# Kernel optimization log

Measured on AMD Instinct MI355X. Metric: run time of the kernel, lower is better.

Reference implementation:

```python
import jax, jax.numpy as jnp
import numpy as np

SAMPLE_RATE = 44100.0
MIN_GAIN, MAX_GAIN = -12.0, 12.0
MIN_Q, MAX_Q = 0.1, 10.0
# (min, max) for the 15 normalized control params, in channel order
PARAM_RANGES = np.array([
    (MIN_GAIN, MAX_GAIN), (20.0, 2000.0), (MIN_Q, MAX_Q),      # low shelf
    (MIN_GAIN, MAX_GAIN), (20.0, 200.0), (MIN_Q, MAX_Q),       # band0 peaking
    (MIN_GAIN, MAX_GAIN), (200.0, 2000.0), (MIN_Q, MAX_Q),     # band1 peaking
    (MIN_GAIN, MAX_GAIN), (2000.0, 12000.0), (MIN_Q, MAX_Q),   # band2 peaking
    (MIN_GAIN, MAX_GAIN), (4000.0, 16000.0), (MIN_Q, MAX_Q),   # high shelf
], dtype=np.float32)


def _biquad(gain_db, f0, q, ftype):
    """RBJ cookbook biquad. Inputs shape (bs,), returns (bs, 6) normalized so a0==1."""
    A = 10.0 ** (gain_db / 40.0)
    w0 = 2.0 * jnp.pi * (f0 / SAMPLE_RATE)
    alpha = jnp.sin(w0) / (2.0 * q)
    cw = jnp.cos(w0)
    sA = jnp.sqrt(A)
    if ftype == 'peaking':
        b0 = 1.0 + alpha * A; b1 = -2.0 * cw; b2 = 1.0 - alpha * A
        a0 = 1.0 + alpha / A; a1 = -2.0 * cw; a2 = 1.0 - alpha / A
    elif ftype == 'low_shelf':
        b0 = A * ((A + 1) - (A - 1) * cw + 2 * sA * alpha)
        b1 = 2 * A * ((A - 1) - (A + 1) * cw)
        b2 = A * ((A + 1) - (A - 1) * cw - 2 * sA * alpha)
        a0 = (A + 1) + (A - 1) * cw + 2 * sA * alpha
        a1 = -2 * ((A - 1) + (A + 1) * cw)
        a2 = (A + 1) + (A - 1) * cw - 2 * sA * alpha
    else:  # high_shelf
        b0 = A * ((A + 1) + (A - 1) * cw + 2 * sA * alpha)
        b1 = -2 * A * ((A - 1) + (A + 1) * cw)
        b2 = A * ((A + 1) + (A - 1) * cw - 2 * sA * alpha)
        a0 = (A + 1) - (A - 1) * cw + 2 * sA * alpha
        a1 = 2 * ((A - 1) - (A + 1) * cw)
        a2 = (A + 1) - (A - 1) * cw - 2 * sA * alpha
    coeffs = jnp.stack([b0, b1, b2, a0, a1, a2], axis=-1)
    return coeffs / a0[..., None]


def _compute_sos(p):
    """p: (bs, 15) denormalized params -> sos (bs, 5, 6)."""
    secs = [
        _biquad(p[:, 0], p[:, 1], p[:, 2], 'low_shelf'),
        _biquad(p[:, 3], p[:, 4], p[:, 5], 'peaking'),
        _biquad(p[:, 6], p[:, 7], p[:, 8], 'peaking'),
        _biquad(p[:, 9], p[:, 10], p[:, 11], 'peaking'),
        _biquad(p[:, 12], p[:, 13], p[:, 14], 'high_shelf'),
    ]
    return jnp.stack(secs, axis=1)


def _sosfilt(sos, x):
    """Cascaded 5-section biquad, direct form II transposed, zero initial state.
    sos: (bs, 5, 6), x: (bs, T) -> (bs, T)."""
    b0, b1, b2 = sos[..., 0], sos[..., 1], sos[..., 2]  # each (bs, 5)
    a1, a2 = sos[..., 4], sos[..., 5]

    def step(carry, xt):
        z1, z2 = carry  # (bs, 5) each
        s = xt  # (bs,)
        z1n, z2n = [], []
        for k in range(5):  # fixed small cascade
            y = b0[:, k] * s + z1[:, k]
            z1n.append(b1[:, k] * s - a1[:, k] * y + z2[:, k])
            z2n.append(b2[:, k] * s - a2[:, k] * y)
            s = y
        return (jnp.stack(z1n, 1), jnp.stack(z2n, 1)), s

    bs = x.shape[0]
    z0 = jnp.zeros((bs, 5), x.dtype)
    _, y = jax.lax.scan(step, (z0, z0), x.T)
    return y.T


def setup_inputs() -> dict:
    key = jax.random.key(0)
    k1, k2 = jax.random.split(key)
    x = jax.random.normal(k1, (32, 1, 131072), dtype=jnp.float32)
    control_params = jax.random.uniform(k2, (32, 15, 1), dtype=jnp.float32)
    return {"x": x, "control_params": control_params}


def reference(x, control_params):
    # denormalize: min + p * (max - min)
    lo = jnp.asarray(PARAM_RANGES[:, 0])
    hi = jnp.asarray(PARAM_RANGES[:, 1])
    p = control_params[:, :, 0]  # (bs, 15)
    p_denorm = lo[None, :] + p * (hi - lo)[None, :]
    sos = _compute_sos(p_denorm)           # (bs, 5, 6)
    y = _sosfilt(sos, x[:, 0, :])          # (bs, T)
    return y[:, None, :], sos
```

## Files before the change

### kernel.cpp

```cpp
#include <hip/hip_runtime.h>
#include <math.h>


#define NB 32
#define LCH 16
#define T_LEN 131072
#define CPB 256
#define BPB 32
#define CCH 8192
#define WPB 128
#define NPOW 13

__constant__ double c_lo[15] = {-12.0,   20.0, 0.1,
                                -12.0,   20.0, 0.1,
                                -12.0,  200.0, 0.1,
                                -12.0, 2000.0, 0.1,
                                -12.0, 4000.0, 0.1};
__constant__ double c_hi[15] = { 12.0,  2000.0, 10.0,
                                 12.0,   200.0, 10.0,
                                 12.0,  2000.0, 10.0,
                                 12.0, 12000.0, 10.0,
                                 12.0, 16000.0, 10.0};

__global__ __launch_bounds__(128)
void eq_setup(const float* __restrict__ cp, float* __restrict__ sos_out,
              float* __restrict__ powers)
{
    int b = blockIdx.x;
    int t = threadIdx.x;
    __shared__ float  sc[5][5];
    __shared__ double Abuf[2][10][10];

    if (t < 5) {
        int k = t;
        double p[3];
#pragma unroll
        for (int j = 0; j < 3; ++j) {
            int i = k * 3 + j;
            double pv = (double)cp[b * 15 + i];
            p[j] = c_lo[i] + pv * (c_hi[i] - c_lo[i]);
        }
        double A     = exp(p[0] * (M_LN10 / 40.0));
        double w0    = 2.0 * M_PI * p[1] / 44100.0;
        double alpha = sin(w0) / (2.0 * p[2]);
        double cw    = cos(w0);
        double sA    = sqrt(A);
        double b0, b1, b2, a0, a1, a2;
        if (k == 0) {
            b0 =     A * ((A + 1) - (A - 1) * cw + 2 * sA * alpha);
            b1 = 2 * A * ((A - 1) - (A + 1) * cw);
            b2 =     A * ((A + 1) - (A - 1) * cw - 2 * sA * alpha);
            a0 =          (A + 1) + (A - 1) * cw + 2 * sA * alpha;
            a1 =    -2 * ((A - 1) + (A + 1) * cw);
            a2 =          (A + 1) + (A - 1) * cw - 2 * sA * alpha;
        } else if (k == 4) {
            b0 =     A * ((A + 1) + (A - 1) * cw + 2 * sA * alpha);
            b1 = -2 * A * ((A - 1) + (A + 1) * cw);
            b2 =     A * ((A + 1) + (A - 1) * cw - 2 * sA * alpha);
            a0 =          (A + 1) - (A - 1) * cw + 2 * sA * alpha;
            a1 =     2 * ((A - 1) - (A + 1) * cw);
            a2 =          (A + 1) - (A - 1) * cw - 2 * sA * alpha;
        } else {
            b0 = 1.0 + alpha * A;
            b1 = -2.0 * cw;
            b2 = 1.0 - alpha * A;
            a0 = 1.0 + alpha / A;
            a1 = -2.0 * cw;
            a2 = 1.0 - alpha / A;
        }
        double inv = 1.0 / a0;
        float fb0 = (float)(b0 * inv), fb1 = (float)(b1 * inv), fb2 = (float)(b2 * inv);
        float fa1 = (float)(a1 * inv), fa2 = (float)(a2 * inv);
        float* o = sos_out + (size_t)(b * 5 + k) * 6;
        o[0] = fb0; o[1] = fb1; o[2] = fb2; o[3] = 1.0f; o[4] = fa1; o[5] = fa2;
        sc[k][0] = fb0; sc[k][1] = fb1; sc[k][2] = fb2; sc[k][3] = fa1; sc[k][4] = fa2;
    }
    __syncthreads();

    if (t < 10) {
        double z[10];
#pragma unroll
        for (int i = 0; i < 10; ++i) z[i] = 0.0;
        z[t] = 1.0;
        double s = 0.0;
        double zn[10];
#pragma unroll
        for (int k = 0; k < 5; ++k) {
            double b0 = sc[k][0], b1 = sc[k][1], b2 = sc[k][2];
            double a1 = sc[k][3], a2 = sc[k][4];
            double y = b0 * s + z[2 * k];
            zn[2 * k]     = b1 * s - a1 * y + z[2 * k + 1];
            zn[2 * k + 1] = b2 * s - a2 * y;
            s = y;
        }
#pragma unroll
        for (int r = 0; r < 10; ++r) Abuf[0][r][t] = zn[r];
    }
    __syncthreads();

    int r = t / 10, cc = t % 10;
    int cur = 0;
    for (int sq = 0; sq < 16; ++sq) {
        double acc = 0.0;
        if (t < 100) {
#pragma unroll
            for (int j = 0; j < 10; ++j) acc += Abuf[cur][r][j] * Abuf[cur][j][cc];
        }
        __syncthreads();
        if (t < 100) Abuf[cur ^ 1][r][cc] = acc;
        __syncthreads();
        cur ^= 1;
        if (sq >= 3 && t < 100) {
            int m = sq - 3;
            powers[((size_t)b * NPOW + m) * 100 + t] = (float)Abuf[cur][r][cc];
        }
    }
}

template<bool ACC>
__device__ __forceinline__ void affineT(const float* __restrict__ P,
                                        const float u[10], float v[10])
{
#pragma unroll
    for (int rr = 0; rr < 10; ++rr) {
        const float* rp = P + rr * 10;
        float a = ACC ? v[rr] : 0.0f;
#pragma unroll
        for (int c = 0; c <= (rr | 1); ++c) a = fmaf(rp[c], u[c], a);
        v[rr] = a;
    }
}

__device__ __forceinline__ void matvecT(const float* __restrict__ P, float v[10])
{
    float u[10];
#pragma unroll
    for (int i = 0; i < 10; ++i) u[i] = v[i];
    affineT<false>(P, u, v);
}

__global__ __launch_bounds__(256, 4)
void eq_pass1(const float* __restrict__ x, const float* __restrict__ sos,
              const float* __restrict__ powers, float* __restrict__ es_g,
              float* __restrict__ wt)
{
    int blk = blockIdx.x;
    int b = blk >> 5, sp = blk & (BPB - 1);
    int tid = threadIdx.x;
    int w = tid >> 6, lw = tid & 63;

    const float* s5 = sos + (size_t)(b * 5) * 6;
    float cb0[5], cb1[5], cb2[5], ca1[5], ca2[5];
#pragma unroll
    for (int k = 0; k < 5; ++k) {
        cb0[k] = s5[k * 6 + 0]; cb1[k] = s5[k * 6 + 1]; cb2[k] = s5[k * 6 + 2];
        ca1[k] = s5[k * 6 + 4]; ca2[k] = s5[k * 6 + 5];
    }

    int c = sp * CPB + tid;
    const float* xp = x + (size_t)b * T_LEN + (size_t)c * LCH;
    float xr[LCH];
#pragma unroll
    for (int t0 = 0; t0 < LCH; t0 += 4) {
        float4 xv = *reinterpret_cast<const float4*>(xp + t0);
        xr[t0] = xv.x; xr[t0 + 1] = xv.y; xr[t0 + 2] = xv.z; xr[t0 + 3] = xv.w;
    }

    float z1[5] = {0, 0, 0, 0, 0}, z2[5] = {0, 0, 0, 0, 0};
#pragma unroll
    for (int j = 0; j < LCH; ++j) {
        float s = xr[j];
#pragma unroll
        for (int k = 0; k < 5; ++k) {
            float yk = fmaf(cb0[k], s, z1[k]);
            float u  = fmaf(cb1[k], s, z2[k]);
            z1[k] = fmaf(-ca1[k], yk, u);
            z2[k] = fmaf(-ca2[k], yk, cb2[k] * s);
            s = yk;
        }
    }
    float sv[10];
#pragma unroll
    for (int k = 0; k < 5; ++k) { sv[2 * k] = z1[k]; sv[2 * k + 1] = z2[k]; }

    const float* Pb = powers + (size_t)b * NPOW * 100;
#pragma unroll
    for (int j = 0; j < 6; ++j) {
        const float* P = Pb + j * 100;
        float u[10];
#pragma unroll
        for (int i = 0; i < 10; ++i) u[i] = __shfl_up(sv[i], 1 << j);
        if (lw >= (1 << j)) affineT<true>(P, u, sv);
    }

    float es[10];
#pragma unroll
    for (int i = 0; i < 10; ++i) es[i] = __shfl_up(sv[i], 1);
    if (lw == 0) {
#pragma unroll
        for (int i = 0; i < 10; ++i) es[i] = 0.0f;
    }
    float* ep = es_g + (size_t)b * 10 * CCH + c;
#pragma unroll
    for (int i = 0; i < 10; ++i) ep[(size_t)i * CCH] = es[i];

    if (lw == 63) {
        int wid = sp * 4 + w;
        float* wp = wt + (size_t)(b * WPB + wid) * 10;
#pragma unroll
        for (int i = 0; i < 10; ++i) wp[i] = sv[i];
    }
}

__global__ __launch_bounds__(64)
void eq_scan(const float* __restrict__ powers, const float* __restrict__ wt,
             float* __restrict__ seeds)
{
    int b = blockIdx.x;
    int l = threadIdx.x;
    const float* Pb = powers + (size_t)b * NPOW * 100;

    const float* wp = wt + (size_t)(b * WPB + 2 * l) * 10;
    float t0[10], t1[10];
#pragma unroll
    for (int i = 0; i < 10; ++i) { t0[i] = wp[i]; t1[i] = wp[10 + i]; }

    float tau[10];
#pragma unroll
    for (int i = 0; i < 10; ++i) tau[i] = t1[i];
    affineT<true>(Pb + 6 * 100, t0, tau);

#pragma unroll
    for (int j = 0; j < 6; ++j) {
        const float* P = Pb + (7 + j) * 100;
        float u[10];
#pragma unroll
        for (int i = 0; i < 10; ++i) u[i] = __shfl_up(tau[i], 1 << j);
        if (l >= (1 << j)) affineT<true>(P, u, tau);
    }

    float e[10];
#pragma unroll
    for (int i = 0; i < 10; ++i) e[i] = __shfl_up(tau[i], 1);
    if (l == 0) {
#pragma unroll
        for (int i = 0; i < 10; ++i) e[i] = 0.0f;
    }

    float s1[10];
#pragma unroll
    for (int i = 0; i < 10; ++i) s1[i] = t0[i];
    affineT<true>(Pb + 6 * 100, e, s1);

    float* sp0 = seeds + (size_t)(b * WPB + 2 * l) * 10;
#pragma unroll
    for (int i = 0; i < 10; ++i) { sp0[i] = e[i]; sp0[10 + i] = s1[i]; }
}

__global__ __launch_bounds__(256, 4)
void eq_pass2(const float* __restrict__ x, const float* __restrict__ sos,
              const float* __restrict__ powers, const float* __restrict__ seeds,
              const float* __restrict__ es_g, float* __restrict__ y)
{
    int blk = blockIdx.x;
    int b = blk >> 5, sp = blk & (BPB - 1);
    int tid = threadIdx.x;
    int w = tid >> 6, lw = tid & 63;

    __shared__ float ys[CPB * 17];

    const float* s5 = sos + (size_t)(b * 5) * 6;
    float cb0[5], cb1[5], cb2[5], ca1[5], ca2[5];
#pragma unroll
    for (int k = 0; k < 5; ++k) {
        cb0[k] = s5[k * 6 + 0]; cb1[k] = s5[k * 6 + 1]; cb2[k] = s5[k * 6 + 2];
        ca1[k] = s5[k * 6 + 4]; ca2[k] = s5[k * 6 + 5];
    }

    int c = sp * CPB + tid;
    const float* xp = x + (size_t)b * T_LEN + (size_t)c * LCH;
    float xr[LCH];
#pragma unroll
    for (int t0 = 0; t0 < LCH; t0 += 4) {
        float4 xv = *reinterpret_cast<const float4*>(xp + t0);
        xr[t0] = xv.x; xr[t0 + 1] = xv.y; xr[t0 + 2] = xv.z; xr[t0 + 3] = xv.w;
    }

    const float* Pb = powers + (size_t)b * NPOW * 100;
    int wid = sp * 4 + w;
    const float* sdp = seeds + (size_t)(b * WPB + wid) * 10;
    float F[10];
#pragma unroll
    for (int i = 0; i < 10; ++i) F[i] = sdp[i];
#pragma unroll
    for (int m = 0; m < 6; ++m) {
        if ((lw >> m) & 1) matvecT(Pb + m * 100, F);
    }

    const float* ep = es_g + (size_t)b * 10 * CCH + c;
    float z1[5], z2[5];
#pragma unroll
    for (int k = 0; k < 5; ++k) {
        z1[k] = F[2 * k]     + ep[(size_t)(2 * k) * CCH];
        z2[k] = F[2 * k + 1] + ep[(size_t)(2 * k + 1) * CCH];
    }

    float* yl = ys + tid * 17;
#pragma unroll
    for (int j = 0; j < LCH; ++j) {
        float s = xr[j];
#pragma unroll
        for (int k = 0; k < 5; ++k) {
            float yk = fmaf(cb0[k], s, z1[k]);
            float u  = fmaf(cb1[k], s, z2[k]);
            z1[k] = fmaf(-ca1[k], yk, u);
            z2[k] = fmaf(-ca2[k], yk, cb2[k] * s);
            s = yk;
        }
        yl[j] = s;
    }
    __syncthreads();

    float* yg = y + (size_t)b * T_LEN + (size_t)sp * (CPB * LCH);
#pragma unroll
    for (int it = 0; it < (CPB * LCH) / (256 * 4); ++it) {
        int i = (tid + it * 256) * 4;
        int p = (i >> 4) * 17 + (i & 15);
        *reinterpret_cast<float4*>(yg + i) =
            make_float4(ys[p], ys[p + 1], ys[p + 2], ys[p + 3]);
    }
}

extern "C" void kernel_launch(void* const* d_in, const int* in_sizes, int n_in,
                              void* d_out, int out_size, void* d_ws, size_t ws_size,
                              hipStream_t stream)
{
    const float* x  = (const float*)d_in[0];
    const float* cp = (const float*)d_in[1];
    float* out = (float*)d_out;
    float* sos = out + (size_t)NB * T_LEN;

    float* powers = (float*)d_ws;
    float* wt     = powers + (size_t)NB * NPOW * 100;
    float* seeds  = wt + (size_t)NB * WPB * 10;
    float* es_g   = seeds + (size_t)NB * WPB * 10;

    eq_setup<<<dim3(NB), dim3(128), 0, stream>>>(cp, sos, powers);
    eq_pass1<<<dim3(NB * BPB), dim3(256), 0, stream>>>(x, sos, powers, es_g, wt);
    eq_scan <<<dim3(NB), dim3(64), 0, stream>>>(powers, wt, seeds);
    eq_pass2<<<dim3(NB * BPB), dim3(256), 0, stream>>>(x, sos, powers, seeds, es_g, out);
}
```

Measured before the change: 45.42 us.

## Fold the cross-warp seed scan into pass2, dropping the scan kernel

Removes the separate eq_scan launch. Every wavefront in eq_pass2 now redundantly computes the 64-lane affine prefix scan over the per-warp transfer states and picks its own seed with a shuffle. This saves one kernel launch and a global round trip for the seeds. In exchange, each of the 1024 blocks repeats the scan work in all four waves, which adds ALU work and register pressure before the filter loop.

```diff
diff --git a/kernel.cpp b/kernel.cpp
--- a/kernel.cpp
+++ b/kernel.cpp
@@ -212,54 +212,9 @@
     }
 }
 
-__global__ __launch_bounds__(64)
-void eq_scan(const float* __restrict__ powers, const float* __restrict__ wt,
-             float* __restrict__ seeds)
-{
-    int b = blockIdx.x;
-    int l = threadIdx.x;
-    const float* Pb = powers + (size_t)b * NPOW * 100;
-
-    const float* wp = wt + (size_t)(b * WPB + 2 * l) * 10;
-    float t0[10], t1[10];
-#pragma unroll
-    for (int i = 0; i < 10; ++i) { t0[i] = wp[i]; t1[i] = wp[10 + i]; }
-
-    float tau[10];
-#pragma unroll
-    for (int i = 0; i < 10; ++i) tau[i] = t1[i];
-    affineT<true>(Pb + 6 * 100, t0, tau);
-
-#pragma unroll
-    for (int j = 0; j < 6; ++j) {
-        const float* P = Pb + (7 + j) * 100;
-        float u[10];
-#pragma unroll
-        for (int i = 0; i < 10; ++i) u[i] = __shfl_up(tau[i], 1 << j);
-        if (l >= (1 << j)) affineT<true>(P, u, tau);
-    }
-
-    float e[10];
-#pragma unroll
-    for (int i = 0; i < 10; ++i) e[i] = __shfl_up(tau[i], 1);
-    if (l == 0) {
-#pragma unroll
-        for (int i = 0; i < 10; ++i) e[i] = 0.0f;
-    }
-
-    float s1[10];
-#pragma unroll
-    for (int i = 0; i < 10; ++i) s1[i] = t0[i];
-    affineT<true>(Pb + 6 * 100, e, s1);
-
-    float* sp0 = seeds + (size_t)(b * WPB + 2 * l) * 10;
-#pragma unroll
-    for (int i = 0; i < 10; ++i) { sp0[i] = e[i]; sp0[10 + i] = s1[i]; }
-}
-
 __global__ __launch_bounds__(256, 4)
 void eq_pass2(const float* __restrict__ x, const float* __restrict__ sos,
-              const float* __restrict__ powers, const float* __restrict__ seeds,
+              const float* __restrict__ powers, const float* __restrict__ wt,
               const float* __restrict__ es_g, float* __restrict__ y)
 {
     int blk = blockIdx.x;
@@ -269,32 +224,65 @@
 
     __shared__ float ys[CPB * 17];
 
+    const float* Pb = powers + (size_t)b * NPOW * 100;
+    int wid = sp * 4 + w;
+
+    const float* wp = wt + (size_t)(b * WPB + 2 * lw) * 10;
+    float t0[10], t1[10];
+#pragma unroll
+    for (int i = 0; i < 10; ++i) { t0[i] = wp[i]; t1[i] = wp[10 + i]; }
+
+    float tau[10];
+#pragma unroll
+    for (int i = 0; i < 10; ++i) tau[i] = t1[i];
+    affineT<true>(Pb + 6 * 100, t0, tau);
+
+#pragma unroll
+    for (int j = 0; j < 6; ++j) {
+        const float* P = Pb + (7 + j) * 100;
+        float u[10];
+#pragma unroll
+        for (int i = 0; i < 10; ++i) u[i] = __shfl_up(tau[i], 1 << j);
+        if (lw >= (1 << j)) affineT<true>(P, u, tau);
+    }
+
+    float e[10];
+#pragma unroll
+    for (int i = 0; i < 10; ++i) e[i] = __shfl_up(tau[i], 1);
+    if (lw == 0) {
+#pragma unroll
+        for (int i = 0; i < 10; ++i) e[i] = 0.0f;
+    }
+    float s1[10];
+#pragma unroll
+    for (int i = 0; i < 10; ++i) s1[i] = t0[i];
+    affineT<true>(Pb + 6 * 100, e, s1);
+
+    float F[10];
+#pragma unroll
+    for (int i = 0; i < 10; ++i)
+        F[i] = __shfl((wid & 1) ? s1[i] : e[i], wid >> 1);
+
+    int c = sp * CPB + tid;
+    const float* xp = x + (size_t)b * T_LEN + (size_t)c * LCH;
+    float xr[LCH];
+#pragma unroll
+    for (int t2 = 0; t2 < LCH; t2 += 4) {
+        float4 xv = *reinterpret_cast<const float4*>(xp + t2);
+        xr[t2] = xv.x; xr[t2 + 1] = xv.y; xr[t2 + 2] = xv.z; xr[t2 + 3] = xv.w;
+    }
+
+#pragma unroll
+    for (int m = 0; m < 6; ++m) {
+        if ((lw >> m) & 1) matvecT(Pb + m * 100, F);
+    }
+
     const float* s5 = sos + (size_t)(b * 5) * 6;
     float cb0[5], cb1[5], cb2[5], ca1[5], ca2[5];
 #pragma unroll
     for (int k = 0; k < 5; ++k) {
         cb0[k] = s5[k * 6 + 0]; cb1[k] = s5[k * 6 + 1]; cb2[k] = s5[k * 6 + 2];
         ca1[k] = s5[k * 6 + 4]; ca2[k] = s5[k * 6 + 5];
-    }
-
-    int c = sp * CPB + tid;
-    const float* xp = x + (size_t)b * T_LEN + (size_t)c * LCH;
-    float xr[LCH];
-#pragma unroll
-    for (int t0 = 0; t0 < LCH; t0 += 4) {
-        float4 xv = *reinterpret_cast<const float4*>(xp + t0);
-        xr[t0] = xv.x; xr[t0 + 1] = xv.y; xr[t0 + 2] = xv.z; xr[t0 + 3] = xv.w;
-    }
-
-    const float* Pb = powers + (size_t)b * NPOW * 100;
-    int wid = sp * 4 + w;
-    const float* sdp = seeds + (size_t)(b * WPB + wid) * 10;
-    float F[10];
-#pragma unroll
-    for (int i = 0; i < 10; ++i) F[i] = sdp[i];
-#pragma unroll
-    for (int m = 0; m < 6; ++m) {
-        if ((lw >> m) & 1) matvecT(Pb + m * 100, F);
     }
 
     const float* ep = es_g + (size_t)b * 10 * CCH + c;
@@ -342,11 +330,9 @@
 
     float* powers = (float*)d_ws;
     float* wt     = powers + (size_t)NB * NPOW * 100;
-    float* seeds  = wt + (size_t)NB * WPB * 10;
-    float* es_g   = seeds + (size_t)NB * WPB * 10;
+    float* es_g   = wt + (size_t)NB * WPB * 10;
 
     eq_setup<<<dim3(NB), dim3(128), 0, stream>>>(cp, sos, powers);
     eq_pass1<<<dim3(NB * BPB), dim3(256), 0, stream>>>(x, sos, powers, es_g, wt);
-    eq_scan <<<dim3(NB), dim3(64), 0, stream>>>(powers, wt, seeds);
-    eq_pass2<<<dim3(NB * BPB), dim3(256), 0, stream>>>(x, sos, powers, seeds, es_g, out);
-}
+    eq_pass2<<<dim3(NB * BPB), dim3(256), 0, stream>>>(x, sos, powers, wt, es_g, out);
+}
```

Measured after the change: 44.51 us. 2.0% less time.
